# Kernel optimization log

Hardware: AMD Instinct MI355X
Metric: run time of the kernel (lower is better)

## Reference

```python
import jax, jax.numpy as jnp
import numpy as np

DN = ('NCHW', 'OIHW', 'NCHW')
NUM_DOMAINS = 4


def conv2d(x, w, pad, groups=1):
    return jax.lax.conv_general_dilated(x, w, (1, 1), pad, dimension_numbers=DN,
                                        feature_group_count=groups)


def batchnorm2d(x, w, b, eps=1e-3):
    m = x.mean(axis=(0, 2, 3), keepdims=True)
    v = x.var(axis=(0, 2, 3), keepdims=True)
    return (x - m) / jnp.sqrt(v + eps) * w[None, :, None, None] + b[None, :, None, None]


def avgpool_w(x, k):
    B, C, H, W = x.shape
    Wo = W // k
    return x[..., :Wo * k].reshape(B, C, H, Wo, k).mean(axis=-1)


def mink(u, v):
    # Minkowski inner product <u,v>_L = -u0*v0 + <us,vs>
    return -u[..., 0] * v[..., 0] + (u[..., 1:] * v[..., 1:]).sum(-1)


def lorentz_elu(x):
    s = jax.nn.elu(x[..., 1:])
    t = jnp.sqrt(1.0 + (s * s).sum(-1, keepdims=True))
    return jnp.concatenate([t, s], -1)


def lorentz_avgpool_w(x, k):
    # (B,H,W,C) Lorentz points; window mean then Lorentz centroid projection
    B, H, W, C = x.shape
    Wo = W // k
    s = x[:, :, :Wo * k].reshape(B, H, Wo, k, C).mean(axis=3)
    d = jnp.sqrt(jnp.clip(jnp.abs(mink(s, s)), 1e-8, None))[..., None]
    return s / d


def lorentz_dbn(x, domains, beta, gamma, eps=1e-5):
    # Domain-specific Riemannian batch norm on the Lorentz manifold (k=1),
    # scalar dispersion (Frechet-mean centroid + geodesic variance per domain).
    B, H, W, C = x.shape
    pts = x.reshape(B, H * W, C)
    npts = float(H * W)
    s = jax.ops.segment_sum(pts.sum(axis=1), domains, num_segments=NUM_DOMAINS)  # (D,C)
    cnt = jax.ops.segment_sum(jnp.full((B,), npts, x.dtype), domains, num_segments=NUM_DOMAINS)
    cnt = jnp.maximum(cnt, 1.0)
    s = s / cnt[:, None]
    mu = s / jnp.sqrt(jnp.clip(jnp.abs(mink(s, s)), 1e-8, None))[:, None]  # (D,C) centroids
    mu_b = mu[domains][:, None, :]                                         # (B,1,C)
    ip = mink(mu_b, pts)                                                   # (B,HW)
    dist = jnp.arccosh(jnp.clip(-ip, 1.0 + 1e-7, None))
    u = pts + ip[..., None] * mu_b
    un = jnp.sqrt(jnp.clip(mink(u, u), 1e-8, None))
    v = dist[..., None] * u / un[..., None]                                # log_mu(x)
    var = jax.ops.segment_sum((dist ** 2).sum(axis=1), domains, num_segments=NUM_DOMAINS) / cnt
    o = jnp.zeros((C,), x.dtype).at[0].set(1.0)
    # parallel transport mu -> origin
    v = v + (-v[..., :1]) / (1.0 + mu_b[..., :1]) * (mu_b + o)
    # rescale by gamma / sqrt(var)
    v = v * (gamma / jnp.sqrt(var[domains] + eps))[:, None, None]
    # parallel transport origin -> beta, then expmap at beta
    v = v + (mink(beta, v) / (1.0 + beta[0]))[..., None] * (o + beta)
    vn = jnp.sqrt(jnp.clip(mink(v, v), 1e-8, None))[..., None]
    y = jnp.cosh(vn) * beta + jnp.sinh(vn) * v / vn
    return y.reshape(B, H, W, C)


def setup_inputs() -> dict:
    key = jax.random.key(0)
    ks = jax.random.split(key, 12)
    B = 128
    d = {}
    d['x'] = jax.random.normal(ks[0], (B, 32, 1024), jnp.float32)
    d['domains'] = jax.random.randint(ks[1], (B,), 0, NUM_DOMAINS, jnp.int32)
    d['conv1_w'] = 0.1 * jax.random.normal(ks[2], (16, 1, 1, 32), jnp.float32)
    d['bn1_w'] = jnp.ones((16,), jnp.float32)
    d['bn1_b'] = jnp.zeros((16,), jnp.float32)
    d['dw_w'] = 0.1 * jax.random.normal(ks[3], (32, 1, 32, 1), jnp.float32)
    d['bn2_w'] = jnp.ones((32,), jnp.float32)
    d['bn2_b'] = jnp.zeros((32,), jnp.float32)
    d['ec1_w'] = 0.1 * jax.random.normal(ks[4], (32, 1, 1, 16), jnp.float32)
    d['b2c1_w'] = 0.1 * jax.random.normal(ks[5], (32, 1, 1, 16), jnp.float32)
    d['b2c2_w'] = 0.1 * jax.random.normal(ks[6], (32, 32, 1, 1), jnp.float32)
    d['bn3_w'] = jnp.ones((32,), jnp.float32)
    d['bn3_b'] = jnp.zeros((32,), jnp.float32)
    d['lc1_w'] = 0.2 * jax.random.normal(ks[7], (33, 33), jnp.float32)
    d['bn_beta'] = jnp.zeros((33,), jnp.float32).at[0].set(1.0)
    d['bn_gamma'] = jnp.ones((1,), jnp.float32)
    d['mlr_a'] = 0.1 * jax.random.normal(ks[8], (1,), jnp.float32)
    d['mlr_z'] = 0.1 * jax.random.normal(ks[9], (1, 512), jnp.float32)
    return d


def reference(x, domains, conv1_w, bn1_w, bn1_b, dw_w, bn2_w, bn2_b, ec1_w,
              b2c1_w, b2c2_w, bn3_w, bn3_b, lc1_w, bn_beta, bn_gamma, mlr_a, mlr_z):
    h = x[:, None]                                       # (B,1,32,1024)
    # block1: temporal conv + BN + depthwise spatial conv + BN + ELU + pool
    h = conv2d(h, conv1_w, ((0, 0), (16, 16)))           # (B,16,32,1025)
    h = batchnorm2d(h, bn1_w, bn1_b)
    h = conv2d(h, dw_w, ((0, 0), (0, 0)), groups=16)     # (B,32,1,1025)
    h = batchnorm2d(h, bn2_w, bn2_b)
    h = jax.nn.elu(h)
    h = avgpool_w(h, 4)                                  # (B,32,1,256)
    # ec1 + block2
    h = conv2d(h, ec1_w, ((0, 0), (8, 8)), groups=32)    # (B,32,1,257)
    h = conv2d(h, b2c1_w, ((0, 0), (8, 8)), groups=32)   # (B,32,1,258)
    h = conv2d(h, b2c2_w, ((0, 0), (0, 0)))              # (B,32,1,258)
    h = batchnorm2d(h, bn3_w, bn3_b)
    h = jax.nn.elu(h)
    h = avgpool_w(h, 4)                                  # (B,32,1,64)
    # to Lorentz: permute, L2-normalize, pad time, projx (time = sqrt(1+|s|^2))
    h = jnp.transpose(h, (0, 2, 3, 1))                   # (B,1,64,32)
    h = h / jnp.clip(jnp.linalg.norm(h, axis=-1, keepdims=True), 1e-12, None)
    t = jnp.sqrt(1.0 + (h * h).sum(-1, keepdims=True))
    h = jnp.concatenate([t, h], -1)                      # (B,1,64,33)
    # LorentzConv2d kernel 1 == Lorentz fully-connected: linear then recompute time
    y = jnp.einsum('bhwc,oc->bhwo', h, lc1_w)
    ys = y[..., 1:]
    yt = jnp.sqrt(1.0 + (ys * ys).sum(-1, keepdims=True))
    h = jnp.concatenate([yt, ys], -1)                    # (B,1,64,33)
    h = lorentz_dbn(h, domains, bn_beta, bn_gamma)
    h = lorentz_elu(h)
    h = lorentz_avgpool_w(h, 4)                          # (B,1,16,33)
    # lorentz_flatten: concat spaces, recompute time -> (B, 16*32+1)
    B = h.shape[0]
    fs = h[..., 1:].reshape(B, -1)
    ft = jnp.sqrt(1.0 + (fs * fs).sum(-1, keepdims=True))
    features = jnp.concatenate([ft, fs], -1)             # (B,513)
    # Lorentz MLR (k=1)
    norm_z = jnp.linalg.norm(mlr_z, axis=-1)             # (1,)
    w_t = jnp.sinh(mlr_a) * norm_z
    bet = jnp.sqrt(jnp.clip(-w_t ** 2 + (jnp.cosh(mlr_a) * norm_z) ** 2, 1e-8, None))
    alpha = -w_t * features[:, :1] + jnp.cosh(mlr_a) * (features[:, 1:] @ mlr_z.T)
    dd = jnp.abs(jnp.arcsinh(alpha / bet))
    logits = jnp.sign(alpha) * bet * dd                  # (B,1)
    return logits.squeeze(-1), features
```

## Files before the change

kernel.cpp:

```cpp
#include <hip/hip_runtime.h>
#include <math.h>

#define Bn 128
#define Hh 32
#define Wx 1024

#define N1f 4198400.0f
#define N2f 131200.0f
#define N3f 33024.0f

#define OFF_EH     33
#define OFF_ET     48
#define OFF_G      64
#define OFF_G2     544
#define OFF_A1     1024
#define OFF_B1     1040
#define OFF_S1_3   1056
#define OFF_S2_3   1088
#define OFF_SEG    1120
#define OFF_CNT    1252
#define OFF_DSQ    1256
#define ZERO_N     1280
#define OFF_PC     2048
#define OFF_PS     34816
#define OFF_PD1    35840
#define OFF_PD2    52224
#define OFF_DWOUT  68608
#define OFF_E2     (68608 + 4194304)
#define OFF_C3     OFF_DWOUT
#define OFF_PTS    (OFF_C3 + 1056768)
#define OFF_VO     (OFF_PTS + 270336)

__device__ __forceinline__ float eluf(float x) { return x > 0.f ? x : expm1f(x); }

__global__ __launch_bounds__(256) void k_edge(const float* __restrict__ x,
                                              float* __restrict__ ws) {
    __shared__ float hd[64 * 48];
    __shared__ float tl[64 * 48];
    int tid = threadIdx.x;
    int r0 = blockIdx.x * 64;
    for (int i = tid; i < 64 * 32; i += 256) {
        int r = i >> 5, c = i & 31;
        tl[r * 48 + 16 + c] = 0.f;
    }
#pragma unroll
    for (int it = 0; it < 4; it++) {
        int idx = tid + it * 256;
        int r = idx >> 4, q = idx & 15;
        const float4* base = (const float4*)(x + (r0 + r) * Wx);
        if (q < 12) ((float4*)(hd + r * 48))[q] = base[q];
        else        ((float4*)(tl + r * 48))[q - 12] = base[252 + (q - 12)];
    }
    __syncthreads();
    for (int p = tid; p < 990; p += 256) {
        float acc = 0.f;
        if (p < 480) {
            int d = p / 15, j = p - d * 15;
            for (int r = 0; r < 64; r++) acc += hd[r * 48 + j] * hd[r * 48 + j + d];
            atomicAdd(&ws[OFF_G + p], acc);
        } else if (p < 960) {
            int p2 = p - 480;
            int d = p2 / 15, j = p2 - d * 15;
            for (int r = 0; r < 64; r++) acc += tl[r * 48 + 1 + j] * tl[r * 48 + 1 + j + d];
            atomicAdd(&ws[OFF_G2 + p2], acc);
        } else {
            int j = p - 960;
            if (j < 15) { for (int r = 0; r < 64; r++) acc += hd[r * 48 + j]; }
            else        { for (int r = 0; r < 64; r++) acc += tl[r * 48 + 1 + (j - 15)]; }
            atomicAdd(&ws[OFF_EH + j], acc);
        }
    }
}

__global__ __launch_bounds__(256, 1) void k_corr(const float* __restrict__ x,
                                                 float* __restrict__ ws) {
    __shared__ float xs[2][1060];
    __shared__ float cacc[32];
    __shared__ float sacc;
    int tid = threadIdx.x;
    if (tid < 32) cacc[tid] = 0.f;
    if (tid == 32) sacc = 0.f;
    for (int i = 1024 + tid; i < 1060; i += 256) { xs[0][i] = 0.f; xs[1][i] = 0.f; }
    float acc[32];
#pragma unroll
    for (int d = 0; d < 32; d++) acc[d] = 0.f;
    float sp = 0.f;
    int r0 = blockIdx.x * 4;
    ((float4*)xs[0])[tid] = ((const float4*)(x + r0 * Wx))[tid];
    __syncthreads();
    for (int rr = 0; rr < 4; rr++) {
        float4 nxt;
        if (rr < 3) nxt = ((const float4*)(x + (r0 + rr + 1) * Wx))[tid];
        const float* bq = xs[rr & 1];
        float v[36];
#pragma unroll
        for (int q = 0; q < 9; q++) {
            float4 t4 = ((const float4*)bq)[tid + q];
            v[4 * q] = t4.x; v[4 * q + 1] = t4.y; v[4 * q + 2] = t4.z; v[4 * q + 3] = t4.w;
        }
#pragma unroll
        for (int i = 0; i < 4; i++) {
            sp += v[i];
#pragma unroll
            for (int d = 0; d < 32; d++) acc[d] += v[i] * v[i + d];
        }
        if (rr < 3) ((float4*)xs[(rr + 1) & 1])[tid] = nxt;
        __syncthreads();
    }
    int lane = tid & 63;
#pragma unroll
    for (int d = 0; d < 32; d++) {
        float vv = acc[d];
#pragma unroll
        for (int off = 32; off > 0; off >>= 1) vv += __shfl_down(vv, off);
        if (lane == 0) atomicAdd(&cacc[d], vv);
    }
    {
        float vv = sp;
#pragma unroll
        for (int off = 32; off > 0; off >>= 1) vv += __shfl_down(vv, off);
        if (lane == 0) atomicAdd(&sacc, vv);
    }
    __syncthreads();
    if (tid < 32) ws[OFF_PC + tid * 1024 + blockIdx.x] = cacc[tid];
    if (tid == 32) ws[OFF_PS + blockIdx.x] = sacc;
}

__global__ __launch_bounds__(512) void k_fold(const float* __restrict__ w1,
                                              const float* __restrict__ bn1w,
                                              const float* __restrict__ bn1b,
                                              float* __restrict__ ws) {
    __shared__ float PH[32][16];
    __shared__ float PT[32][16];
    __shared__ float Ts[32];
    __shared__ float w1s[512];
    __shared__ float sumsq[16];
    __shared__ float meanv[16];
    __shared__ float Cs[32];
    __shared__ float sS[16];
    int tid = threadIdx.x;
    w1s[tid] = w1[tid];
    if (tid < 16) sumsq[tid] = 0.f;
    {
        int d = tid >> 4, i = tid & 15;
        const float4* pc = (const float4*)(ws + OFF_PC + d * 1024 + i * 64);
        float s = 0.f;
#pragma unroll
        for (int k = 0; k < 16; k++) { float4 t4 = pc[k]; s += t4.x + t4.y + t4.z + t4.w; }
        s += __shfl_down(s, 8); s += __shfl_down(s, 4);
        s += __shfl_down(s, 2); s += __shfl_down(s, 1);
        if (i == 0) Cs[d] = s;
    }
    __syncthreads();
    if (tid < 32) {
        int d = tid;
        float s = 0.f;
        for (int j = 0; j < 15; j++) { s += ws[OFF_G + d * 15 + j]; PH[d][j] = s; }
        float s2 = 0.f;
        for (int j = 14; j >= 0; j--) { s2 += ws[OFF_G2 + d * 15 + j]; PT[d][j] = s2; }
    } else if (tid < 48) {
        int i = tid - 32;
        const float4* ps = (const float4*)(ws + OFF_PS + i * 64);
        float s = 0.f;
#pragma unroll
        for (int k = 0; k < 16; k++) { float4 t4 = ps[k]; s += t4.x + t4.y + t4.z + t4.w; }
        sS[i] = s;
    }
    __syncthreads();
    if (tid >= 64 && tid < 96) {
        int k = tid - 64;
        float S = 0.f;
        for (int j = 0; j < 16; j++) S += sS[j];
        float t = S;
        for (int j = 0; j <= k - 17; j++) t -= ws[OFF_EH + j];
        if (k <= 14) for (int j = k; j < 15; j++) t -= ws[OFF_ET + j];
        Ts[k] = t;
    }
    __syncthreads();
    int c = tid >> 5, d = tid & 31;
    float Cd = Cs[d];
    float part = 0.f;
    for (int k = 0; k + d < 32; k++) {
        float head = (k >= 17) ? PH[d][k - 17] : 0.f;
        float tail = (k <= 14) ? PT[d][k] : 0.f;
        float R = Cd - head - tail;
        part += w1s[c * 32 + k] * w1s[c * 32 + k + d] * R;
    }
    if (d > 0) part *= 2.f;
    atomicAdd(&sumsq[c], part);
    if (d == 0) {
        float mp = 0.f;
        for (int k = 0; k < 32; k++) mp += w1s[c * 32 + k] * Ts[k];
        meanv[c] = mp / N1f;
    }
    __syncthreads();
    if (tid < 16) {
        float mean = meanv[tid];
        float var = fmaxf(sumsq[tid] / N1f - mean * mean, 0.f);
        float a = bn1w[tid] / sqrtf(var + 1e-3f);
        ws[OFF_A1 + tid] = a;
        ws[OFF_B1 + tid] = bn1b[tid] - mean * a;
    }
}

__global__ __launch_bounds__(256, 2) void k_dw(const float* __restrict__ x,
                                               const float* __restrict__ w1,
                                               const float* __restrict__ dww,
                                               float* __restrict__ ws) {
    __shared__ float xs[32 * 288];
    __shared__ float Ys[32 * 288];
    __shared__ float dws[1024];
    __shared__ float w1s[512];
    __shared__ float a1s[16], b1s[16], Dv[32];
    int tid = threadIdx.x;
    int b = blockIdx.x;
    int z = blockIdx.y;
    int wt0 = z * 256;
    for (int i = tid; i < 1024; i += 256) dws[i] = dww[i];
    w1s[tid] = w1[tid];
    w1s[256 + tid] = w1[256 + tid];
    if (tid < 16) { a1s[tid] = ws[OFF_A1 + tid]; b1s[tid] = ws[OFF_B1 + tid]; }
    const float* xb = x + b * (Hh * Wx);
    for (int i = tid; i < 32 * 288; i += 256) {
        int h = i / 288, cc = i - h * 288;
        int gc = wt0 - 16 + cc;
        xs[i] = (gc >= 0 && gc < Wx) ? xb[h * Wx + gc] : 0.f;
    }
    __syncthreads();
    if (tid < 32) {
        float d = 0.f;
        for (int h = 0; h < 32; h++) d += dws[tid * 32 + h];
        Dv[tid] = d;
    }
#pragma unroll
    for (int pass = 0; pass < 2; pass++) {
        int p = pass * 256 + tid;
        if (p < 288) {
            float xv[32];
#pragma unroll
            for (int h = 0; h < 32; h++) xv[h] = xs[h * 288 + p];
#pragma unroll
            for (int ocb = 0; ocb < 4; ocb++) {
                const float4* d4 = (const float4*)(dws + ocb * 256);
                float acc[8];
#pragma unroll
                for (int j = 0; j < 8; j++) acc[j] = 0.f;
#pragma unroll
                for (int j = 0; j < 8; j++) {
#pragma unroll
                    for (int hq = 0; hq < 8; hq++) {
                        float4 dv = d4[j * 8 + hq];
                        acc[j] += xv[4 * hq] * dv.x + xv[4 * hq + 1] * dv.y +
                                  xv[4 * hq + 2] * dv.z + xv[4 * hq + 3] * dv.w;
                    }
                }
#pragma unroll
                for (int j = 0; j < 8; j++) Ys[(ocb * 8 + j) * 288 + p] = acc[j];
            }
        }
    }
    __syncthreads();
    int wq = tid & 63;
    int wave = tid >> 6;
    int oc0 = wave * 8;
    float ls1[8], ls2[8];
#pragma unroll
    for (int j = 0; j < 8; j++) { ls1[j] = 0.f; ls2[j] = 0.f; }
#pragma unroll
    for (int gp = 0; gp < 4; gp++) {
        int g = wave * 4 + gp;
        float wr[32];
        const float4* wg = (const float4*)(w1s + g * 32);
#pragma unroll
        for (int q = 0; q < 8; q++) {
            float4 t4 = wg[q];
            wr[4 * q] = t4.x; wr[4 * q + 1] = t4.y; wr[4 * q + 2] = t4.z; wr[4 * q + 3] = t4.w;
        }
        float ag = a1s[g], bg = b1s[g];
#pragma unroll
        for (int jj = 0; jj < 2; jj++) {
            int j = gp * 2 + jj;
            int oc = oc0 + j;
            float y[36];
            const float4* yq = (const float4*)(Ys + oc * 288 + 4 * wq);
#pragma unroll
            for (int q = 0; q < 9; q++) {
                float4 t4 = yq[q];
                y[4 * q] = t4.x; y[4 * q + 1] = t4.y; y[4 * q + 2] = t4.z; y[4 * q + 3] = t4.w;
            }
            float bb = bg * Dv[oc];
            float ov[4];
#pragma unroll
            for (int m = 0; m < 4; m++) {
                float s = 0.f;
#pragma unroll
                for (int k = 0; k < 32; k++) s += wr[k] * y[m + k];
                float val = ag * s + bb;
                ov[m] = val;
                ls1[j] += val; ls2[j] += val * val;
            }
            *((float4*)(ws + OFF_DWOUT + (b * 32 + oc) * 1024 + wt0 + 4 * wq)) =
                make_float4(ov[0], ov[1], ov[2], ov[3]);
            if (z == 3 && wq == 63) {
                float s = 0.f;
#pragma unroll
                for (int k = 0; k < 32; k++) s += wr[k] * Ys[oc * 288 + 256 + k];
                float val = ag * s + bb;
                ls1[j] += val; ls2[j] += val * val;
            }
        }
    }
#pragma unroll
    for (int j = 0; j < 8; j++) {
#pragma unroll
        for (int off = 32; off > 0; off >>= 1) {
            ls1[j] += __shfl_down(ls1[j], off);
            ls2[j] += __shfl_down(ls2[j], off);
        }
    }
    if (wq == 0) {
#pragma unroll
        for (int j = 0; j < 8; j++) {
            ws[OFF_PD1 + (oc0 + j) * 512 + z * 128 + b] = ls1[j];
            ws[OFF_PD2 + (oc0 + j) * 512 + z * 128 + b] = ls2[j];
        }
    }
}

__global__ __launch_bounds__(64) void k_pe(const float* __restrict__ ec1w,
                                           const float* __restrict__ bc1w,
                                           const float* __restrict__ bn2w,
                                           const float* __restrict__ bn2b,
                                           float* __restrict__ ws) {
    __shared__ float ins[272];
    __shared__ float e1p[288];
    int b = blockIdx.x, c = blockIdx.y;
    int t = threadIdx.x;
    if (t < 8) { ins[t] = 0.f; ins[264 + t] = 0.f; e1p[t] = 0.f; }
    if (t < 23) e1p[265 + t] = 0.f;
    const float4* p1 = (const float4*)(ws + OFF_PD1 + c * 512);
    const float4* p2 = (const float4*)(ws + OFF_PD2 + c * 512);
    float4 a0 = p1[t * 2], a1 = p1[t * 2 + 1], c0 = p2[t * 2], c1 = p2[t * 2 + 1];
    float s1 = a0.x + a0.y + a0.z + a0.w + a1.x + a1.y + a1.z + a1.w;
    float s2 = c0.x + c0.y + c0.z + c0.w + c1.x + c1.y + c1.z + c1.w;
#pragma unroll
    for (int off = 32; off > 0; off >>= 1) {
        s1 += __shfl_xor(s1, off);
        s2 += __shfl_xor(s2, off);
    }
    float mean = s1 / N2f;
    float var = fmaxf(s2 / N2f - mean * mean, 0.f);
    float a = bn2w[c] / sqrtf(var + 1e-3f);
    float bb = bn2b[c] - mean * a;
    const float4* dr = (const float4*)(ws + OFF_DWOUT + (b * 32 + c) * 1024);
#pragma unroll
    for (int q = 0; q < 4; q++) {
        float4 v4 = dr[q * 64 + t];
        ins[8 + q * 64 + t] = 0.25f * (eluf(a * v4.x + bb) + eluf(a * v4.y + bb) +
                                       eluf(a * v4.z + bb) + eluf(a * v4.w + bb));
    }
    __syncthreads();
    float ek[16], bk[16];
#pragma unroll
    for (int k = 0; k < 16; k++) { ek[k] = ec1w[c * 16 + k]; bk[k] = bc1w[c * 16 + k]; }
    for (int w = t; w < 257; w += 64) {
        float s = 0.f;
#pragma unroll
        for (int k = 0; k < 16; k++) s += ins[w + k] * ek[k];
        e1p[8 + w] = s;
    }
    __syncthreads();
    float* e2r = ws + OFF_E2 + (b * 32 + c) * 258;
    for (int w = t; w < 258; w += 64) {
        float s = 0.f;
#pragma unroll
        for (int k = 0; k < 16; k++) s += e1p[w + k] * bk[k];
        e2r[w] = s;
    }
}

__global__ __launch_bounds__(256) void k_sep2(const float* __restrict__ bc2w,
                                              float* __restrict__ ws) {
    __shared__ float es[32 * 129];
    __shared__ float bs[1056];
    int b = blockIdx.x;
    int wb = blockIdx.y * 129;
    int t = threadIdx.x;
    for (int i = t; i < 1024; i += 256) { int o = i >> 5, cc = i & 31; bs[o * 33 + cc] = bc2w[i]; }
    const float* e2b = ws + OFF_E2 + b * 8256;
    for (int i = t; i < 4128; i += 256) {
        int cc = i / 129, wl = i - cc * 129;
        es[i] = e2b[cc * 258 + wb + wl];
    }
    __syncthreads();
    int o = t >> 3, w0 = t & 7;
    float wr[32];
#pragma unroll
    for (int cc = 0; cc < 32; cc++) wr[cc] = bs[o * 33 + cc];
    float s1 = 0.f, s2 = 0.f;
    float* c3r = ws + OFF_C3 + (b * 32 + o) * 258 + wb;
    for (int wl = w0; wl < 129; wl += 8) {
        float s = 0.f;
#pragma unroll
        for (int cc = 0; cc < 32; cc++) s += es[cc * 129 + wl] * wr[cc];
        c3r[wl] = s;
        s1 += s; s2 += s * s;
    }
    s1 += __shfl_down(s1, 4, 8); s1 += __shfl_down(s1, 2, 8); s1 += __shfl_down(s1, 1, 8);
    s2 += __shfl_down(s2, 4, 8); s2 += __shfl_down(s2, 2, 8); s2 += __shfl_down(s2, 1, 8);
    if (w0 == 0) {
        atomicAdd(&ws[OFF_S1_3 + o], s1);
        atomicAdd(&ws[OFF_S2_3 + o], s2);
    }
}

__global__ __launch_bounds__(256, 1) void k_head(const float* __restrict__ bn3w,
                                                 const float* __restrict__ bn3b,
                                                 const float* __restrict__ lc1w,
                                                 const int* __restrict__ domains,
                                                 float* __restrict__ ws) {
    __shared__ float q[2048];
    __shared__ float lc1s[1089];
    __shared__ float psum[33];
    __shared__ float ssyp[4][64];
    __shared__ float a3s[32], b3s[32];
    int tid = threadIdx.x;
    int b = blockIdx.x;
    if (tid < 32) {
        float mean = ws[OFF_S1_3 + tid] / N3f;
        float var = fmaxf(ws[OFF_S2_3 + tid] / N3f - mean * mean, 0.f);
        float a = bn3w[tid] / sqrtf(var + 1e-3f);
        a3s[tid] = a;
        b3s[tid] = bn3b[tid] - mean * a;
    }
    for (int i = tid; i < 1089; i += 256) lc1s[i] = lc1w[i];
    __syncthreads();
    const float* c3 = ws + OFF_C3 + b * 8256;
    for (int idx = tid; idx < 2048; idx += 256) {
        int c = idx >> 6, wp = idx & 63;
        float a = a3s[c], bb = b3s[c];
        float acc = 0.f;
#pragma unroll
        for (int j = 0; j < 4; j++) {
            float e = a * c3[c * 258 + wp * 4 + j] + bb;
            acc += eluf(e);
        }
        q[idx] = 0.25f * acc;
    }
    __syncthreads();
    int w = tid & 63, sub = tid >> 6;
    float qv[32];
    float ssq = 0.f;
#pragma unroll
    for (int c = 0; c < 32; c++) { qv[c] = q[c * 64 + w]; ssq += qv[c] * qv[c]; }
    float inv = 1.f / fmaxf(sqrtf(ssq), 1e-12f);
    float ss2 = 0.f;
#pragma unroll
    for (int c = 0; c < 32; c++) { qv[c] *= inv; ss2 += qv[c] * qv[c]; }
    float t = sqrtf(1.f + ss2);
    int o0 = 1 + sub * 8;
    float p[8];
    float ssy_part = 0.f;
#pragma unroll
    for (int i = 0; i < 8; i++) {
        int o = o0 + i;
        float s = lc1s[o * 33] * t;
#pragma unroll
        for (int c = 0; c < 32; c++) s += lc1s[o * 33 + 1 + c] * qv[c];
        p[i] = s;
        ssy_part += s * s;
    }
    ssyp[sub][w] = ssy_part;
    float* pr = ws + OFF_PTS + (b * 64 + w) * 33;
#pragma unroll
    for (int i = 0; i < 8; i++) pr[o0 + i] = p[i];
    __syncthreads();
    float yt = 0.f;
    if (sub == 0) {
        float ssy = ssyp[0][w] + ssyp[1][w] + ssyp[2][w] + ssyp[3][w];
        yt = sqrtf(1.f + ssy);
        pr[0] = yt;
    }
#pragma unroll
    for (int i = 0; i < 8; i++) {
        float vv = p[i];
#pragma unroll
        for (int off = 32; off > 0; off >>= 1) vv += __shfl_down(vv, off);
        if (w == 0) psum[o0 + i] = vv;
    }
    {
        float vv = yt;
#pragma unroll
        for (int off = 32; off > 0; off >>= 1) vv += __shfl_down(vv, off);
        if (w == 0 && sub == 0) psum[0] = vv;
    }
    __syncthreads();
    int dom = domains[b];
    if (tid < 33) atomicAdd(&ws[OFF_SEG + dom * 33 + tid], psum[tid]);
    if (tid == 64) atomicAdd(&ws[OFF_CNT + dom], 64.f);
}

__global__ __launch_bounds__(64, 1) void k_tangent(const int* __restrict__ domains,
                                                   float* __restrict__ ws) {
    int b = blockIdx.x;
    int w = threadIdx.x;
    int dom = domains[b];
    float cnt = fmaxf(ws[OFF_CNT + dom], 1.f);
    float m[33];
    float s0 = ws[OFF_SEG + dom * 33] / cnt;
    m[0] = s0;
    float msum = 0.f;
#pragma unroll
    for (int c = 1; c < 33; c++) {
        m[c] = ws[OFF_SEG + dom * 33 + c] / cnt;
        msum += m[c] * m[c];
    }
    float mkm = -s0 * s0 + msum;
    float dn = 1.f / sqrtf(fmaxf(fabsf(mkm), 1e-8f));
#pragma unroll
    for (int c = 0; c < 33; c++) m[c] *= dn;
    const float* pr = ws + OFF_PTS + (b * 64 + w) * 33;
    float p[33];
#pragma unroll
    for (int c = 0; c < 33; c++) p[c] = pr[c];
    float ip = -m[0] * p[0];
#pragma unroll
    for (int c = 1; c < 33; c++) ip += m[c] * p[c];
    float z = fmaxf(-ip, 1.f + 1e-7f);
    float dist = acoshf(z);
    float u[33];
#pragma unroll
    for (int c = 0; c < 33; c++) u[c] = p[c] + ip * m[c];
    float mk = -u[0] * u[0];
#pragma unroll
    for (int c = 1; c < 33; c++) mk += u[c] * u[c];
    float un = sqrtf(fmaxf(mk, 1e-8f));
    float r = dist / un;
    float v0 = r * u[0];
    float coef = -v0 / (1.f + m[0]);
    float* vo = ws + OFF_VO + (b * 64 + w) * 33;
    vo[0] = v0 + coef * (m[0] + 1.f);
#pragma unroll
    for (int c = 1; c < 33; c++) vo[c] = r * u[c] + coef * m[c];
    float dsq = dist * dist;
#pragma unroll
    for (int off = 32; off > 0; off >>= 1) dsq += __shfl_down(dsq, off);
    if (w == 0) atomicAdd(&ws[OFF_DSQ + dom], dsq);
}

__global__ __launch_bounds__(64, 1) void k_final(const int* __restrict__ domains,
                                                 const float* __restrict__ beta,
                                                 const float* __restrict__ gamma,
                                                 const float* __restrict__ mlr_a,
                                                 const float* __restrict__ mlr_z,
                                                 float* __restrict__ ws,
                                                 float* __restrict__ out) {
    __shared__ float he[64 * 33];
    __shared__ float hp[16 * 33];
    int b = blockIdx.x;
    int w = threadIdx.x;
    int dom = domains[b];
    float cnt = fmaxf(ws[OFF_CNT + dom], 1.f);
    float var = ws[OFF_DSQ + dom] / cnt;
    float sc = gamma[0] / sqrtf(var + 1e-5f);
    float bt[33];
#pragma unroll
    for (int c = 0; c < 33; c++) bt[c] = beta[c];
    const float* vo = ws + OFF_VO + (b * 64 + w) * 33;
    float v[33];
#pragma unroll
    for (int c = 0; c < 33; c++) v[c] = vo[c] * sc;
    float mb = -bt[0] * v[0];
#pragma unroll
    for (int c = 1; c < 33; c++) mb += bt[c] * v[c];
    float coef = mb / (1.f + bt[0]);
    v[0] += coef * (1.f + bt[0]);
#pragma unroll
    for (int c = 1; c < 33; c++) v[c] += coef * bt[c];
    float mk = -v[0] * v[0];
#pragma unroll
    for (int c = 1; c < 33; c++) mk += v[c] * v[c];
    float vn = sqrtf(fmaxf(mk, 1e-8f));
    float ch = coshf(vn), sh = sinhf(vn) / vn;
    float ss = 0.f;
#pragma unroll
    for (int c = 1; c < 33; c++) {
        float y = ch * bt[c] + sh * v[c];
        float s = eluf(y);
        he[w * 33 + c] = s;
        ss += s * s;
    }
    he[w * 33] = sqrtf(1.f + ss);
    __syncthreads();
    if (w < 16) {
        float tmp[33];
        float mk2;
        {
            float a0 = 0.25f * (he[(4 * w) * 33] + he[(4 * w + 1) * 33] +
                                he[(4 * w + 2) * 33] + he[(4 * w + 3) * 33]);
            tmp[0] = a0;
            mk2 = -a0 * a0;
        }
#pragma unroll
        for (int c = 1; c < 33; c++) {
            float a = 0.25f * (he[(4 * w) * 33 + c] + he[(4 * w + 1) * 33 + c] +
                               he[(4 * w + 2) * 33 + c] + he[(4 * w + 3) * 33 + c]);
            tmp[c] = a;
            mk2 += a * a;
        }
        float dd = sqrtf(fmaxf(fabsf(mk2), 1e-8f));
#pragma unroll
        for (int c = 0; c < 33; c++) hp[w * 33 + c] = tmp[c] / dd;
    }
    __syncthreads();
    float ssq = 0.f, sdz = 0.f, zz = 0.f;
    for (int j = w; j < 512; j += 64) {
        float val = hp[(j >> 5) * 33 + 1 + (j & 31)];
        float zv = mlr_z[j];
        ssq += val * val;
        sdz += val * zv;
        zz += zv * zv;
        out[128 + b * 513 + 1 + j] = val;
    }
#pragma unroll
    for (int off = 32; off > 0; off >>= 1) {
        ssq += __shfl_down(ssq, off);
        sdz += __shfl_down(sdz, off);
        zz += __shfl_down(zz, off);
    }
    if (w == 0) {
        float nz = sqrtf(zz);
        float a = mlr_a[0];
        float cha = coshf(a);
        float wt = sinhf(a) * nz;
        float cn = cha * nz;
        float bet = sqrtf(fmaxf(cn * cn - wt * wt, 1e-8f));
        float ft = sqrtf(1.f + ssq);
        float alpha = -wt * ft + cha * sdz;
        out[128 + b * 513] = ft;
        out[b] = bet * asinhf(alpha / bet);
    }
}

extern "C" void kernel_launch(void* const* d_in, const int* in_sizes, int n_in,
                              void* d_out, int out_size, void* d_ws, size_t ws_size,
                              hipStream_t stream) {
    const float* x       = (const float*)d_in[0];
    const int*   domains = (const int*)d_in[1];
    const float* conv1_w = (const float*)d_in[2];
    const float* bn1_w   = (const float*)d_in[3];
    const float* bn1_b   = (const float*)d_in[4];
    const float* dw_w    = (const float*)d_in[5];
    const float* bn2_w   = (const float*)d_in[6];
    const float* bn2_b   = (const float*)d_in[7];
    const float* ec1_w   = (const float*)d_in[8];
    const float* b2c1_w  = (const float*)d_in[9];
    const float* b2c2_w  = (const float*)d_in[10];
    const float* bn3_w   = (const float*)d_in[11];
    const float* bn3_b   = (const float*)d_in[12];
    const float* lc1_w   = (const float*)d_in[13];
    const float* bn_beta = (const float*)d_in[14];
    const float* bn_gamma= (const float*)d_in[15];
    const float* mlr_a   = (const float*)d_in[16];
    const float* mlr_z   = (const float*)d_in[17];
    float* out = (float*)d_out;
    float* ws  = (float*)d_ws;

    hipMemsetAsync(ws, 0, ZERO_N * sizeof(float), stream);
    k_edge<<<64, 256, 0, stream>>>(x, ws);
    k_corr<<<1024, 256, 0, stream>>>(x, ws);
    k_fold<<<1, 512, 0, stream>>>(conv1_w, bn1_w, bn1_b, ws);
    k_dw<<<dim3(128, 4), 256, 0, stream>>>(x, conv1_w, dw_w, ws);
    k_pe<<<dim3(128, 32), 64, 0, stream>>>(ec1_w, b2c1_w, bn2_w, bn2_b, ws);
    k_sep2<<<dim3(128, 2), 256, 0, stream>>>(b2c2_w, ws);
    k_head<<<Bn, 256, 0, stream>>>(bn3_w, bn3_b, lc1_w, domains, ws);
    k_tangent<<<Bn, 64, 0, stream>>>(domains, ws);
    k_final<<<Bn, 64, 0, stream>>>(domains, bn_beta, bn_gamma, mlr_a, mlr_z, ws, out);
}
```

Baseline: 237.1 us.

## Halve k_dw width tile, reuse one shared buffer, double grid and occupancy

The depthwise/pointwise kernel now processes 128 output columns per block instead of 256. It reuses a single shared buffer for both the input tile and the intermediate result, and launches 8 column tiles per batch with a target of 4 blocks per SM. The first stage is restructured so each of 160 threads computes all 32 channels in registers. Partial BN statistics are reduced per half-wave, and the partial-sum layout is widened to 1024 entries per channel, with k_pe updated to read it. The aim is more parallelism and less LDS per block. The trade-off is more halo recomputation, higher register pressure from the 32-wide accumulator, and more partial sums to reduce.

```diff
diff --git a/kernel.cpp b/kernel.cpp
--- a/kernel.cpp
+++ b/kernel.cpp
@@ -24,9 +24,9 @@
 #define OFF_PC     2048
 #define OFF_PS     34816
 #define OFF_PD1    35840
-#define OFF_PD2    52224
-#define OFF_DWOUT  68608
-#define OFF_E2     (68608 + 4194304)
+#define OFF_PD2    68608
+#define OFF_DWOUT  101376
+#define OFF_E2     (101376 + 4194304)
 #define OFF_C3     OFF_DWOUT
 #define OFF_PTS    (OFF_C3 + 1056768)
 #define OFF_VO     (OFF_PTS + 270336)
@@ -203,28 +203,27 @@
     }
 }
 
-__global__ __launch_bounds__(256, 2) void k_dw(const float* __restrict__ x,
+__global__ __launch_bounds__(256, 4) void k_dw(const float* __restrict__ x,
                                                const float* __restrict__ w1,
                                                const float* __restrict__ dww,
                                                float* __restrict__ ws) {
-    __shared__ float xs[32 * 288];
-    __shared__ float Ys[32 * 288];
+    __shared__ float buf[32 * 160];
     __shared__ float dws[1024];
     __shared__ float w1s[512];
     __shared__ float a1s[16], b1s[16], Dv[32];
     int tid = threadIdx.x;
     int b = blockIdx.x;
     int z = blockIdx.y;
-    int wt0 = z * 256;
+    int wt0 = z * 128;
     for (int i = tid; i < 1024; i += 256) dws[i] = dww[i];
     w1s[tid] = w1[tid];
     w1s[256 + tid] = w1[256 + tid];
     if (tid < 16) { a1s[tid] = ws[OFF_A1 + tid]; b1s[tid] = ws[OFF_B1 + tid]; }
     const float* xb = x + b * (Hh * Wx);
-    for (int i = tid; i < 32 * 288; i += 256) {
-        int h = i / 288, cc = i - h * 288;
+    for (int i = tid; i < 32 * 160; i += 256) {
+        int h = i / 160, cc = i - h * 160;
         int gc = wt0 - 16 + cc;
-        xs[i] = (gc >= 0 && gc < Wx) ? xb[h * Wx + gc] : 0.f;
+        buf[i] = (gc >= 0 && gc < Wx) ? xb[h * Wx + gc] : 0.f;
     }
     __syncthreads();
     if (tid < 32) {
@@ -232,43 +231,32 @@
         for (int h = 0; h < 32; h++) d += dws[tid * 32 + h];
         Dv[tid] = d;
     }
-#pragma unroll
-    for (int pass = 0; pass < 2; pass++) {
-        int p = pass * 256 + tid;
-        if (p < 288) {
-            float xv[32];
-#pragma unroll
-            for (int h = 0; h < 32; h++) xv[h] = xs[h * 288 + p];
-#pragma unroll
-            for (int ocb = 0; ocb < 4; ocb++) {
-                const float4* d4 = (const float4*)(dws + ocb * 256);
-                float acc[8];
-#pragma unroll
-                for (int j = 0; j < 8; j++) acc[j] = 0.f;
-#pragma unroll
-                for (int j = 0; j < 8; j++) {
-#pragma unroll
-                    for (int hq = 0; hq < 8; hq++) {
-                        float4 dv = d4[j * 8 + hq];
-                        acc[j] += xv[4 * hq] * dv.x + xv[4 * hq + 1] * dv.y +
-                                  xv[4 * hq + 2] * dv.z + xv[4 * hq + 3] * dv.w;
-                    }
-                }
-#pragma unroll
-                for (int j = 0; j < 8; j++) Ys[(ocb * 8 + j) * 288 + p] = acc[j];
-            }
-        }
-    }
-    __syncthreads();
-    int wq = tid & 63;
+    float acc[32];
+    if (tid < 160) {
+        float xv[32];
+#pragma unroll
+        for (int h = 0; h < 32; h++) xv[h] = buf[h * 160 + tid];
+#pragma unroll
+        for (int oc = 0; oc < 32; oc++) acc[oc] = 0.f;
+#pragma unroll
+        for (int h = 0; h < 32; h++) {
+#pragma unroll
+            for (int oc = 0; oc < 32; oc++) acc[oc] += xv[h] * dws[oc * 32 + h];
+        }
+    }
+    __syncthreads();
+    if (tid < 160) {
+#pragma unroll
+        for (int oc = 0; oc < 32; oc++) buf[oc * 160 + tid] = acc[oc];
+    }
+    __syncthreads();
+    int lane = tid & 63;
     int wave = tid >> 6;
-    int oc0 = wave * 8;
-    float ls1[8], ls2[8];
-#pragma unroll
-    for (int j = 0; j < 8; j++) { ls1[j] = 0.f; ls2[j] = 0.f; }
-#pragma unroll
-    for (int gp = 0; gp < 4; gp++) {
-        int g = wave * 4 + gp;
+    int half = lane >> 5;
+    int qw = lane & 31;
+    for (int pass = 0; pass < 4; pass++) {
+        int oc = pass * 8 + wave * 2 + half;
+        int g = oc >> 1;
         float wr[32];
         const float4* wg = (const float4*)(w1s + g * 32);
 #pragma unroll
@@ -276,53 +264,42 @@
             float4 t4 = wg[q];
             wr[4 * q] = t4.x; wr[4 * q + 1] = t4.y; wr[4 * q + 2] = t4.z; wr[4 * q + 3] = t4.w;
         }
-        float ag = a1s[g], bg = b1s[g];
-#pragma unroll
-        for (int jj = 0; jj < 2; jj++) {
-            int j = gp * 2 + jj;
-            int oc = oc0 + j;
-            float y[36];
-            const float4* yq = (const float4*)(Ys + oc * 288 + 4 * wq);
-#pragma unroll
-            for (int q = 0; q < 9; q++) {
-                float4 t4 = yq[q];
-                y[4 * q] = t4.x; y[4 * q + 1] = t4.y; y[4 * q + 2] = t4.z; y[4 * q + 3] = t4.w;
-            }
-            float bb = bg * Dv[oc];
-            float ov[4];
-#pragma unroll
-            for (int m = 0; m < 4; m++) {
-                float s = 0.f;
-#pragma unroll
-                for (int k = 0; k < 32; k++) s += wr[k] * y[m + k];
-                float val = ag * s + bb;
-                ov[m] = val;
-                ls1[j] += val; ls2[j] += val * val;
-            }
-            *((float4*)(ws + OFF_DWOUT + (b * 32 + oc) * 1024 + wt0 + 4 * wq)) =
-                make_float4(ov[0], ov[1], ov[2], ov[3]);
-            if (z == 3 && wq == 63) {
-                float s = 0.f;
-#pragma unroll
-                for (int k = 0; k < 32; k++) s += wr[k] * Ys[oc * 288 + 256 + k];
-                float val = ag * s + bb;
-                ls1[j] += val; ls2[j] += val * val;
-            }
-        }
-    }
-#pragma unroll
-    for (int j = 0; j < 8; j++) {
-#pragma unroll
-        for (int off = 32; off > 0; off >>= 1) {
-            ls1[j] += __shfl_down(ls1[j], off);
-            ls2[j] += __shfl_down(ls2[j], off);
-        }
-    }
-    if (wq == 0) {
-#pragma unroll
-        for (int j = 0; j < 8; j++) {
-            ws[OFF_PD1 + (oc0 + j) * 512 + z * 128 + b] = ls1[j];
-            ws[OFF_PD2 + (oc0 + j) * 512 + z * 128 + b] = ls2[j];
+        float ag = a1s[g], bb = b1s[g] * Dv[oc];
+        float y[36];
+        const float4* yq = (const float4*)(buf + oc * 160 + 4 * qw);
+#pragma unroll
+        for (int q = 0; q < 9; q++) {
+            float4 t4 = yq[q];
+            y[4 * q] = t4.x; y[4 * q + 1] = t4.y; y[4 * q + 2] = t4.z; y[4 * q + 3] = t4.w;
+        }
+        float ls1 = 0.f, ls2 = 0.f;
+        float ov[4];
+#pragma unroll
+        for (int m = 0; m < 4; m++) {
+            float s = 0.f;
+#pragma unroll
+            for (int k = 0; k < 32; k++) s += wr[k] * y[m + k];
+            float val = ag * s + bb;
+            ov[m] = val;
+            ls1 += val; ls2 += val * val;
+        }
+        *((float4*)(ws + OFF_DWOUT + (b * 32 + oc) * 1024 + wt0 + 4 * qw)) =
+            make_float4(ov[0], ov[1], ov[2], ov[3]);
+        if (z == 7 && qw == 0) {
+            float s = 0.f;
+#pragma unroll
+            for (int k = 0; k < 32; k++) s += wr[k] * buf[oc * 160 + 128 + k];
+            float val = ag * s + bb;
+            ls1 += val; ls2 += val * val;
+        }
+#pragma unroll
+        for (int off = 16; off > 0; off >>= 1) {
+            ls1 += __shfl_down(ls1, off, 32);
+            ls2 += __shfl_down(ls2, off, 32);
+        }
+        if (qw == 0) {
+            ws[OFF_PD1 + oc * 1024 + z * 128 + b] = ls1;
+            ws[OFF_PD2 + oc * 1024 + z * 128 + b] = ls2;
         }
     }
 }
@@ -338,11 +315,16 @@
     int t = threadIdx.x;
     if (t < 8) { ins[t] = 0.f; ins[264 + t] = 0.f; e1p[t] = 0.f; }
     if (t < 23) e1p[265 + t] = 0.f;
-    const float4* p1 = (const float4*)(ws + OFF_PD1 + c * 512);
-    const float4* p2 = (const float4*)(ws + OFF_PD2 + c * 512);
-    float4 a0 = p1[t * 2], a1 = p1[t * 2 + 1], c0 = p2[t * 2], c1 = p2[t * 2 + 1];
-    float s1 = a0.x + a0.y + a0.z + a0.w + a1.x + a1.y + a1.z + a1.w;
-    float s2 = c0.x + c0.y + c0.z + c0.w + c1.x + c1.y + c1.z + c1.w;
+    const float4* p1 = (const float4*)(ws + OFF_PD1 + c * 1024);
+    const float4* p2 = (const float4*)(ws + OFF_PD2 + c * 1024);
+    float s1 = 0.f, s2 = 0.f;
+#pragma unroll
+    for (int q = 0; q < 4; q++) {
+        float4 a4 = p1[t * 4 + q];
+        float4 c4 = p2[t * 4 + q];
+        s1 += a4.x + a4.y + a4.z + a4.w;
+        s2 += c4.x + c4.y + c4.z + c4.w;
+    }
 #pragma unroll
     for (int off = 32; off > 0; off >>= 1) {
         s1 += __shfl_xor(s1, off);
@@ -670,7 +652,7 @@
     k_edge<<<64, 256, 0, stream>>>(x, ws);
     k_corr<<<1024, 256, 0, stream>>>(x, ws);
     k_fold<<<1, 512, 0, stream>>>(conv1_w, bn1_w, bn1_b, ws);
-    k_dw<<<dim3(128, 4), 256, 0, stream>>>(x, conv1_w, dw_w, ws);
+    k_dw<<<dim3(128, 8), 256, 0, stream>>>(x, conv1_w, dw_w, ws);
     k_pe<<<dim3(128, 32), 64, 0, stream>>>(ec1_w, b2c1_w, bn2_w, bn2_b, ws);
     k_sep2<<<dim3(128, 2), 256, 0, stream>>>(b2c2_w, ws);
     k_head<<<Bn, 256, 0, stream>>>(bn3_w, bn3_b, lc1_w, domains, ws);
```

Result: slower. 258.3 us (+8.9%).
